# Kernel tuning notes

Measured on AMD Instinct MI355X. Metric: run time of the kernel, lower is better.

## Reference

```python
import jax, jax.numpy as jnp
import numpy as np

N_AGENTS = 12
N_THREADS = 4096
DIM = 3
N_VEC = 4
HID = 64
INV_NF = 32
LAYERS = 2
N = N_THREADS * N_AGENTS


def _intra_graph_edges():
    # fully-connected directed edges within each env's agent graph
    i, j = np.meshgrid(np.arange(N_AGENTS), np.arange(N_AGENTS), indexing='ij')
    mask = i != j
    ri, ci = i[mask], j[mask]  # [132]
    off = (np.arange(N_THREADS) * N_AGENTS)[:, None]
    row = (ri[None, :] + off).reshape(-1).astype(np.int32)
    col = (ci[None, :] + off).reshape(-1).astype(np.int32)
    return jnp.asarray(row), jnp.asarray(col)


def setup_inputs() -> dict:
    key = jax.random.key(0)
    ks = jax.random.split(key, 16)
    s = 0.05
    row, col = _intra_graph_edges()
    return {
        'h0': jax.random.normal(ks[0], (N, INV_NF), jnp.float32),
        'x0': jax.random.normal(ks[1], (N, DIM, N_VEC), jnp.float32),
        'W_embed': jax.random.normal(ks[2], (INV_NF, HID), jnp.float32) * s,
        'b_embed': jnp.zeros((HID,), jnp.float32),
        'We1': jax.random.normal(ks[3], (LAYERS, 2 * HID + N_VEC, HID), jnp.float32) * s,
        'be1': jnp.zeros((LAYERS, HID), jnp.float32),
        'We2': jax.random.normal(ks[4], (LAYERS, HID, HID), jnp.float32) * s,
        'be2': jnp.zeros((LAYERS, HID), jnp.float32),
        'Wx': jax.random.normal(ks[5], (LAYERS, HID, N_VEC), jnp.float32) * s,
        'bx': jnp.zeros((LAYERS, N_VEC), jnp.float32),
        'Wh1': jax.random.normal(ks[6], (LAYERS, 2 * HID, HID), jnp.float32) * s,
        'bh1': jnp.zeros((LAYERS, HID), jnp.float32),
        'Wh2': jax.random.normal(ks[7], (LAYERS, HID, HID), jnp.float32) * s,
        'bh2': jnp.zeros((LAYERS, HID), jnp.float32),
        'w_act': jax.random.normal(ks[8], (N_VEC,), jnp.float32) * s,
        'log_std': jnp.full((DIM,), -0.5, jnp.float32),
        'row': row,
        'col': col,
    }


def reference(h0, x0, W_embed, b_embed, We1, be1, We2, be2, Wx, bx,
              Wh1, bh1, Wh2, bh2, w_act, log_std, row, col):
    silu = jax.nn.silu
    n = h0.shape[0]
    h = h0 @ W_embed + b_embed            # node embedding, [N, HID]
    x = x0                                 # equivariant features, [N, DIM, N_VEC]
    deg = jnp.maximum(jax.ops.segment_sum(jnp.ones_like(row, jnp.float32), row, num_segments=n), 1.0)
    for l in range(LAYERS):
        hi, hj = h[row], h[col]
        diff = x[row] - x[col]                        # [E, DIM, N_VEC]
        radial = jnp.sum(diff * diff, axis=1)          # [E, N_VEC]
        m = silu(jnp.concatenate([hi, hj, radial], -1) @ We1[l] + be1[l])
        m = silu(m @ We2[l] + be2[l])                  # edge messages [E, HID]
        wc = m @ Wx[l] + bx[l]                         # per-vector coord weights [E, N_VEC]
        x = x + jax.ops.segment_sum(diff * wc[:, None, :], row, num_segments=n) / deg[:, None, None]
        agg = jax.ops.segment_sum(m, row, num_segments=n)
        h = h + silu(jnp.concatenate([h, agg], -1) @ Wh1[l] + bh1[l]) @ Wh2[l] + bh2[l]
    mu = jnp.einsum('ndv,v->nd', x, w_act)             # act_net: Linear(N_VEC,1,bias=False)
    actions = mu                                        # deterministic: mode of Normal(mu, std)
    log_probs = jnp.broadcast_to(-log_std - 0.5 * jnp.log(2.0 * jnp.pi), mu.shape)
    actions = actions.reshape(N_THREADS, N_AGENTS, DIM)
    log_probs = log_probs.reshape(N_THREADS, N_AGENTS, DIM)
    return actions, log_probs
```

## Files before the change

### kernel.cpp

```cpp
#include <hip/hip_runtime.h>

#define NAG 12
#define NTH 4096
#define NEDGE 132
#define ENVW 2
#define NWAVE 4
#define LDB 72
#define LDT 20

typedef __bf16 bf16_8 __attribute__((ext_vector_type(8)));
typedef __bf16 bf16_4 __attribute__((ext_vector_type(4)));
typedef float  f32x4  __attribute__((ext_vector_type(4)));

#define MFMA(a,b,c) __builtin_amdgcn_mfma_f32_16x16x32_bf16((a),(b),(c),0,0,0)

#define WS_FRAGS 100
#define WS_BIAS_F32 25600
#define WS_BX_F32   27648
#define WS_BYTES 111104

__device__ __forceinline__ float silu_f(float z) {
    float e = __expf(-z);
    return z * __builtin_amdgcn_rcpf(1.0f + e);
}

__device__ __forceinline__ bf16_8 loadB64(const float* __restrict__ W, int kbase, int n, int q) {
    bf16_8 b;
    #pragma unroll
    for (int j = 0; j < 8; ++j) b[j] = (__bf16)W[(kbase + q*8 + j) * 64 + n];
    return b;
}

__device__ __forceinline__ bf16_8 packA8(const float* S) {
    f32x4 u = *(const f32x4*)S, v = *(const f32x4*)(S + 4);
    bf16_8 a;
    a[0]=(__bf16)u.x; a[1]=(__bf16)u.y; a[2]=(__bf16)u.z; a[3]=(__bf16)u.w;
    a[4]=(__bf16)v.x; a[5]=(__bf16)v.y; a[6]=(__bf16)v.z; a[7]=(__bf16)v.w;
    return a;
}

__global__ __launch_bounds__(64) void prep_frags(
    const float* __restrict__ W_embed, const float* __restrict__ We1,
    const float* __restrict__ We2, const float* __restrict__ Wh1,
    const float* __restrict__ Wh2,
    const float* __restrict__ be1, const float* __restrict__ be2,
    const float* __restrict__ bh1, const float* __restrict__ bh2,
    const float* __restrict__ bx, __bf16* __restrict__ wsb)
{
    const int f = blockIdx.x, lane = threadIdx.x;
    const int q = lane >> 4, n16 = lane & 15;
    float* wsf = (float*)wsb;
    if (f < WS_FRAGS) {
        const float* src; int kbase, nbase;
        if (f < 4) { src = W_embed; kbase = 0; nbase = f * 16; }
        else {
            int g0 = f - 4, l = g0 / 48, r = g0 % 48;
            if      (r < 8)  { int nt=r>>1, kh=r&1;            src = We1 + l*NEDGE*64; kbase = kh*32;      nbase = nt*16; }
            else if (r < 16) { int rr=r-8,  nt=rr>>1, kh=rr&1; src = We1 + l*NEDGE*64; kbase = 64 + kh*32; nbase = nt*16; }
            else if (r < 24) { int rr=r-16, nt=rr>>1, kh=rr&1; src = We2 + l*64*64;    kbase = kh*32;      nbase = nt*16; }
            else if (r < 40) { int rr=r-24, nt=rr>>2, ks=rr&3; src = Wh1 + l*128*64;   kbase = ks*32;      nbase = nt*16; }
            else             { int rr=r-40, nt=rr>>1, kh=rr&1; src = Wh2 + l*64*64;    kbase = kh*32;      nbase = nt*16; }
        }
        bf16_8 b = loadB64(src, kbase, nbase + n16, q);
        *(bf16_8*)(wsb + (size_t)f * 512 + lane * 8) = b;
    } else if (f < WS_FRAGS + 8) {
        int f2 = f - WS_FRAGS, l = f2 >> 2, w = f2 & 3;
        const float* src = (w == 0 ? be1 : w == 1 ? be2 : w == 2 ? bh1 : bh2) + l * 64;
        f32x4 v = { src[n16], src[16 + n16], src[32 + n16], src[48 + n16] };
        *(f32x4*)(wsf + WS_BIAS_F32 + ((size_t)(l*4 + w) * 64 + lane) * 4) = v;
    } else {
        #pragma unroll
        for (int l = 0; l < 2; ++l)
            wsf[WS_BX_F32 + l*64 + lane] = (n16 < 4) ? bx[l*4 + n16] : 0.f;
    }
}

template<bool WS>
__device__ __forceinline__ bf16_8 frg(const __bf16* __restrict__ wsb, int fid,
                                      const float* __restrict__ src, int kbase, int n, int lane) {
    if (WS) return *(const bf16_8*)(wsb + (size_t)fid * 512 + lane * 8);
    else    return loadB64(src, kbase, n, (lane >> 4));
}

template<bool WS>
__global__ void __launch_bounds__(64 * NWAVE) egnn11(
    const float* __restrict__ h0, const float* __restrict__ x0,
    const float* __restrict__ W_embed, const float* __restrict__ b_embed,
    const float* __restrict__ We1, const float* __restrict__ be1,
    const float* __restrict__ We2, const float* __restrict__ be2,
    const float* __restrict__ Wx, const float* __restrict__ bx,
    const float* __restrict__ Wh1, const float* __restrict__ bh1,
    const float* __restrict__ Wh2, const float* __restrict__ bh2,
    const float* __restrict__ w_act, const float* __restrict__ log_std,
    const __bf16* __restrict__ wsb, float* __restrict__ out)
{
    __shared__ __align__(16) __bf16 sh  [NWAVE][ENVW][NAG * LDB];
    __shared__ __align__(16) __bf16 sHa [NWAVE][ENVW][NAG * LDB];
    __shared__ __align__(16) __bf16 sHb [NWAVE][ENVW][NAG * LDB];
    __shared__ __align__(16) __bf16 mstT[NWAVE][ENVW][64 * LDT];
    __shared__ __align__(16) float  sx  [NWAVE][ENVW][NAG * 16];
    __shared__ __align__(16) __bf16 sWcB[NWAVE][ENVW][NEDGE * 4];
    __shared__ __align__(16) float  sWb [NWAVE][4 * 64];

    const int tid  = threadIdx.x;
    const int wv   = tid >> 6;
    const int lane = tid & 63;
    const int q = lane >> 4, n16 = lane & 15;
    const int rowA = (n16 < NAG) ? n16 : (NAG - 1);
    const int env0 = (blockIdx.x * NWAVE + wv) * ENVW;
    const float* wsf = (const float*)wsb;

    if (lane < NAG * 3) {
        int d = lane % 3;
        float lp = -log_std[d] - 0.9189385332046727f;
        #pragma unroll
        for (int ep = 0; ep < ENVW; ++ep)
            out[NTH * NAG * 3 + (env0 + ep) * (NAG*3) + lane] = lp;
    }

    #pragma unroll
    for (int p = 0; p < (ENVW * 144 + 63) / 64; ++p) {
        int idx = p * 64 + lane;
        if (idx < ENVW * 144) {
            int ep = idx / 144, r2 = idx - ep * 144;
            sx[wv][ep][(r2 / 12) * 16 + r2 % 12] = x0[(env0) * NAG * 12 + idx];
        }
    }

    f32x4 hC[ENVW][4];
    {
        bf16_8 a[ENVW];
        #pragma unroll
        for (int ep = 0; ep < ENVW; ++ep)
            a[ep] = packA8(h0 + ((env0 + ep) * NAG + rowA) * 32 + q * 8);
        #pragma unroll
        for (int nt = 0; nt < 4; ++nt) {
            bf16_8 b = frg<WS>(wsb, nt, W_embed, 0, nt*16 + n16, lane);
            float bias = b_embed[nt*16 + n16];
            #pragma unroll
            for (int ep = 0; ep < ENVW; ++ep) {
                f32x4 acc = {0.f,0.f,0.f,0.f};
                acc = MFMA(a[ep], b, acc);
                #pragma unroll
                for (int r = 0; r < 4; ++r) acc[r] += bias;
                hC[ep][nt] = acc;
            }
        }
        #pragma unroll
        for (int ep = 0; ep < ENVW; ++ep)
            #pragma unroll
            for (int nt = 0; nt < 4; ++nt)
                #pragma unroll
                for (int r = 0; r < 4; ++r) {
                    int row = q*4 + r;
                    if (row < NAG) sh[wv][ep][row*LDB + nt*16 + n16] = (__bf16)hC[ep][nt][r];
                }
    }

    #pragma unroll 1
    for (int l = 0; l < 2; ++l) {
        const float* We1l = We1 + l * NEDGE * 64;
        const float* be1l = be1 + l * 64;
        const float* be2l = be2 + l * 64;
        const float* Wxl  = Wx  + l * 64 * 4;
        const float* bxl  = bx  + l * 4;
        const float* We2l = We2 + l * 64 * 64;
        const float* Wh1l = Wh1 + l * 128 * 64;
        const float* bh1l = bh1 + l * 64;
        const float* Wh2l = Wh2 + l * 64 * 64;
        const float* bh2l = bh2 + l * 64;
        const int L = 4 + l * 48;

        f32x4 be1q, be2q, bh1q, bh2q;
        float bxv;
        if (WS) {
            const float* bb = wsf + WS_BIAS_F32 + (size_t)(l*4) * 256 + lane * 4;
            be1q = *(const f32x4*)(bb);
            be2q = *(const f32x4*)(bb + 256);
            bh1q = *(const f32x4*)(bb + 512);
            bh2q = *(const f32x4*)(bb + 768);
            bxv  = wsf[WS_BX_F32 + l*64 + lane];
        } else {
            #pragma unroll
            for (int nt = 0; nt < 4; ++nt) {
                be1q[nt] = be1l[nt*16+n16]; be2q[nt] = be2l[nt*16+n16];
                bh1q[nt] = bh1l[nt*16+n16]; bh2q[nt] = bh2l[nt*16+n16];
            }
            bxv = (n16 < 4) ? bxl[n16] : 0.f;
        }

        {
            bf16_8 a0[ENVW], a1[ENVW];
            #pragma unroll
            for (int ep = 0; ep < ENVW; ++ep) {
                a0[ep] = *(const bf16_8*)(sh[wv][ep] + rowA*LDB + q*8);
                a1[ep] = *(const bf16_8*)(sh[wv][ep] + rowA*LDB + 32 + q*8);
            }
            #pragma unroll
            for (int nt = 0; nt < 4; ++nt) {
                bf16_8 b0 = frg<WS>(wsb, L+nt*2+0,   We1l, 0,  nt*16+n16, lane);
                bf16_8 b1 = frg<WS>(wsb, L+nt*2+1,   We1l, 32, nt*16+n16, lane);
                bf16_8 c0 = frg<WS>(wsb, L+8+nt*2+0, We1l, 64, nt*16+n16, lane);
                bf16_8 c1 = frg<WS>(wsb, L+8+nt*2+1, We1l, 96, nt*16+n16, lane);
                #pragma unroll
                for (int ep = 0; ep < ENVW; ++ep) {
                    f32x4 aA = {0.f,0.f,0.f,0.f}, aB = {0.f,0.f,0.f,0.f};
                    aA = MFMA(a0[ep], b0, aA); aA = MFMA(a1[ep], b1, aA);
                    aB = MFMA(a0[ep], c0, aB); aB = MFMA(a1[ep], c1, aB);
                    #pragma unroll
                    for (int r = 0; r < 4; ++r) {
                        int row = q*4 + r;
                        if (row < NAG) {
                            sHa[wv][ep][row*LDB + nt*16+n16] = (__bf16)(aA[r] + be1q[nt]);
                            sHb[wv][ep][row*LDB + nt*16+n16] = (__bf16)aB[r];
                        }
                    }
                }
            }
        }
        #pragma unroll
        for (int p = 0; p < 4; ++p) sWb[wv][p*64 + lane] = We1l[(128+p)*64 + lane];

        float agg[ENVW][NAG];
        #pragma unroll
        for (int ep = 0; ep < ENVW; ++ep)
            #pragma unroll
            for (int i = 0; i < NAG; ++i) agg[ep][i] = 0.f;
        bf16_8 w2f[4][2], wxf[2];
        #pragma unroll
        for (int nt = 0; nt < 4; ++nt) {
            w2f[nt][0] = frg<WS>(wsb, L+16+nt*2+0, We2l, 0,  nt*16+n16, lane);
            w2f[nt][1] = frg<WS>(wsb, L+16+nt*2+1, We2l, 32, nt*16+n16, lane);
        }
        #pragma unroll
        for (int kh = 0; kh < 2; ++kh) {
            bf16_8 b;
            #pragma unroll
            for (int j2 = 0; j2 < 8; ++j2)
                b[j2] = (n16 < 4) ? (__bf16)Wxl[(kh*32 + q*8 + j2)*4 + n16] : (__bf16)0.f;
            wxf[kh] = b;
        }

        #pragma unroll
        for (int t = 0; t < 9; ++t) {
            const int e  = t*16 + n16;
            const int ec = (e < NEDGE) ? e : (NEDGE - 1);
            const int i  = ec / 11;
            const int jj = ec - i * 11;
            const int j  = jj + (jj >= i);
            bf16_8 af[ENVW][2];
            #pragma unroll
            for (int ep = 0; ep < ENVW; ++ep) {
                f32x4 rd = {0.f,0.f,0.f,0.f};
                #pragma unroll
                for (int d = 0; d < 3; ++d) {
                    f32x4 xi = *(const f32x4*)(sx[wv][ep] + i*16 + d*4);
                    f32x4 xj = *(const f32x4*)(sx[wv][ep] + j*16 + d*4);
                    f32x4 df = xi - xj;
                    rd += df * df;
                }
                #pragma unroll
                for (int kh = 0; kh < 2; ++kh) {
                    const int cb = kh*32 + q*8;
                    bf16_8 ha = *(const bf16_8*)(sHa[wv][ep] + i*LDB + cb);
                    bf16_8 hb = *(const bf16_8*)(sHb[wv][ep] + j*LDB + cb);
                    f32x4 wr0 = {0.f,0.f,0.f,0.f}, wr1 = {0.f,0.f,0.f,0.f};
                    #pragma unroll
                    for (int v = 0; v < 4; ++v) {
                        f32x4 wa = *(const f32x4*)(sWb[wv] + v*64 + cb);
                        f32x4 wb = *(const f32x4*)(sWb[wv] + v*64 + cb + 4);
                        wr0 += rd[v] * wa; wr1 += rd[v] * wb;
                    }
                    bf16_8 a;
                    #pragma unroll
                    for (int c = 0; c < 4; ++c)
                        a[c]   = (__bf16)silu_f((float)ha[c]   + (float)hb[c]   + wr0[c]);
                    #pragma unroll
                    for (int c = 0; c < 4; ++c)
                        a[4+c] = (__bf16)silu_f((float)ha[4+c] + (float)hb[4+c] + wr1[c]);
                    af[ep][kh] = a;
                }
            }
            #pragma unroll
            for (int ep = 0; ep < ENVW; ++ep) {
                __bf16* mT = &mstT[wv][ep][0];
                #pragma unroll
                for (int nt = 0; nt < 4; ++nt) {
                    f32x4 acc = {0.f,0.f,0.f,0.f};
                    acc = MFMA(af[ep][0], w2f[nt][0], acc);
                    acc = MFMA(af[ep][1], w2f[nt][1], acc);
                    bf16_4 mv;
                    #pragma unroll
                    for (int r = 0; r < 4; ++r) mv[r] = (__bf16)silu_f(acc[r] + be2q[nt]);
                    *(bf16_4*)(mT + (nt*16 + n16)*LDT + q*4) = mv;
                }
            }
            #pragma unroll
            for (int ep = 0; ep < ENVW; ++ep) {
                const __bf16* mT = &mstT[wv][ep][0];
                bf16_8 aw0, aw1;
                #pragma unroll
                for (int j2 = 0; j2 < 8; ++j2) {
                    aw0[j2] = mT[(q*8 + j2)*LDT + n16];
                    aw1[j2] = mT[(32 + q*8 + j2)*LDT + n16];
                }
                f32x4 acc = {0.f,0.f,0.f,0.f};
                acc = MFMA(aw0, wxf[0], acc);
                acc = MFMA(aw1, wxf[1], acc);
                if (n16 < 4) {
                    #pragma unroll
                    for (int r = 0; r < 4; ++r) {
                        int row = t*16 + q*4 + r;
                        if (row < NEDGE) sWcB[wv][ep][row*4 + n16] = (__bf16)(acc[r] + bxv);
                    }
                }
            }
            #pragma unroll
            for (int ep = 0; ep < ENVW; ++ep) {
                const __bf16* mT = &mstT[wv][ep][0];
                bf16_4 c0 = *(const bf16_4*)(mT + lane*LDT + 0);
                #pragma unroll
                for (int el = 0; el < 4; ++el) agg[ep][(t*16 + el)/11] += (float)c0[el];
                if (t < 8) {
                    bf16_4 c1 = *(const bf16_4*)(mT + lane*LDT + 4);
                    bf16_4 c2 = *(const bf16_4*)(mT + lane*LDT + 8);
                    bf16_4 c3 = *(const bf16_4*)(mT + lane*LDT + 12);
                    #pragma unroll
                    for (int el = 0; el < 4; ++el) {
                        agg[ep][(t*16 + 4  + el)/11] += (float)c1[el];
                        agg[ep][(t*16 + 8  + el)/11] += (float)c2[el];
                        agg[ep][(t*16 + 12 + el)/11] += (float)c3[el];
                    }
                }
            }
        }
        #pragma unroll
        for (int ep = 0; ep < ENVW; ++ep)
            #pragma unroll
            for (int i = 0; i < NAG; ++i) sHb[wv][ep][i*LDB + lane] = (__bf16)agg[ep][i];

        float xn[ENVW][3];
        #pragma unroll
        for (int p = 0; p < 3; ++p) {
            int idx = p*64 + lane;
            int xi = idx / 12, dv = idx % 12, v = dv & 3;
            bool act = idx < 144;
            int xic = act ? xi : 0;
            #pragma unroll
            for (int ep = 0; ep < ENVW; ++ep) {
                float xiv = sx[wv][ep][xic*16 + dv];
                float acc = 0.f;
                #pragma unroll
                for (int j2 = 0; j2 < NAG; ++j2) {
                    int e2 = xic*11 + j2 - (j2 > xic ? 1 : 0);
                    e2 = (e2 < NEDGE) ? e2 : (NEDGE - 1);
                    float term = (xiv - sx[wv][ep][j2*16 + dv]) * (float)sWcB[wv][ep][e2*4 + v];
                    acc += (j2 == xic) ? 0.f : term;
                }
                xn[ep][p] = act ? (xiv + acc * (1.0f / 11.0f)) : 0.f;
            }
        }
        {
            bf16_8 ah0[ENVW], ah1[ENVW], ag0[ENVW], ag1[ENVW];
            #pragma unroll
            for (int ep = 0; ep < ENVW; ++ep) {
                ah0[ep] = *(const bf16_8*)(sh[wv][ep]  + rowA*LDB + q*8);
                ah1[ep] = *(const bf16_8*)(sh[wv][ep]  + rowA*LDB + 32 + q*8);
                ag0[ep] = *(const bf16_8*)(sHb[wv][ep] + rowA*LDB + q*8);
                ag1[ep] = *(const bf16_8*)(sHb[wv][ep] + rowA*LDB + 32 + q*8);
            }
            #pragma unroll
            for (int nt = 0; nt < 4; ++nt) {
                bf16_8 b0 = frg<WS>(wsb, L+24+nt*4+0, Wh1l, 0,  nt*16+n16, lane);
                bf16_8 b1 = frg<WS>(wsb, L+24+nt*4+1, Wh1l, 32, nt*16+n16, lane);
                bf16_8 b2 = frg<WS>(wsb, L+24+nt*4+2, Wh1l, 64, nt*16+n16, lane);
                bf16_8 b3 = frg<WS>(wsb, L+24+nt*4+3, Wh1l, 96, nt*16+n16, lane);
                #pragma unroll
                for (int ep = 0; ep < ENVW; ++ep) {
                    f32x4 acc = {0.f,0.f,0.f,0.f};
                    acc = MFMA(ah0[ep], b0, acc); acc = MFMA(ah1[ep], b1, acc);
                    acc = MFMA(ag0[ep], b2, acc); acc = MFMA(ag1[ep], b3, acc);
                    #pragma unroll
                    for (int r = 0; r < 4; ++r) {
                        int row = q*4 + r;
                        if (row < NAG) sHa[wv][ep][row*LDB + nt*16+n16] = (__bf16)silu_f(acc[r] + bh1q[nt]);
                    }
                }
            }
        }
        #pragma unroll
        for (int p = 0; p < 3; ++p) {
            int idx = p*64 + lane;
            if (idx < 144) {
                #pragma unroll
                for (int ep = 0; ep < ENVW; ++ep)
                    sx[wv][ep][(idx/12)*16 + idx%12] = xn[ep][p];
            }
        }
        {
            bf16_8 at0[ENVW], at1[ENVW];
            #pragma unroll
            for (int ep = 0; ep < ENVW; ++ep) {
                at0[ep] = *(const bf16_8*)(sHa[wv][ep] + rowA*LDB + q*8);
                at1[ep] = *(const bf16_8*)(sHa[wv][ep] + rowA*LDB + 32 + q*8);
            }
            #pragma unroll
            for (int nt = 0; nt < 4; ++nt) {
                bf16_8 b0 = frg<WS>(wsb, L+40+nt*2+0, Wh2l, 0,  nt*16+n16, lane);
                bf16_8 b1 = frg<WS>(wsb, L+40+nt*2+1, Wh2l, 32, nt*16+n16, lane);
                #pragma unroll
                for (int ep = 0; ep < ENVW; ++ep) {
                    f32x4 acc = {0.f,0.f,0.f,0.f};
                    acc = MFMA(at0[ep], b0, acc);
                    acc = MFMA(at1[ep], b1, acc);
                    #pragma unroll
                    for (int r = 0; r < 4; ++r) hC[ep][nt][r] += acc[r] + bh2q[nt];
                }
            }
            #pragma unroll
            for (int ep = 0; ep < ENVW; ++ep)
                #pragma unroll
                for (int nt = 0; nt < 4; ++nt)
                    #pragma unroll
                    for (int r = 0; r < 4; ++r) {
                        int row = q*4 + r;
                        if (row < NAG) sh[wv][ep][row*LDB + nt*16+n16] = (__bf16)hC[ep][nt][r];
                    }
        }
    }

    if (lane < NAG * 3) {
        int i = lane / 3, d = lane - i * 3;
        #pragma unroll
        for (int ep = 0; ep < ENVW; ++ep) {
            float mu = 0.f;
            #pragma unroll
            for (int v = 0; v < 4; ++v) mu += sx[wv][ep][i*16 + d*4 + v] * w_act[v];
            out[(env0 + ep) * (NAG*3) + lane] = mu;
        }
    }
}

extern "C" void kernel_launch(void* const* d_in, const int* in_sizes, int n_in,
                              void* d_out, int out_size, void* d_ws, size_t ws_size,
                              hipStream_t stream) {
    const float* h0   = (const float*)d_in[0];
    const float* x0   = (const float*)d_in[1];
    const float* Wem  = (const float*)d_in[2];
    const float* bem  = (const float*)d_in[3];
    const float* We1  = (const float*)d_in[4];
    const float* be1  = (const float*)d_in[5];
    const float* We2  = (const float*)d_in[6];
    const float* be2  = (const float*)d_in[7];
    const float* Wx   = (const float*)d_in[8];
    const float* bx   = (const float*)d_in[9];
    const float* Wh1  = (const float*)d_in[10];
    const float* bh1  = (const float*)d_in[11];
    const float* Wh2  = (const float*)d_in[12];
    const float* bh2  = (const float*)d_in[13];
    const float* wact = (const float*)d_in[14];
    const float* lstd = (const float*)d_in[15];
    float* out = (float*)d_out;

    if (ws_size >= (size_t)WS_BYTES) {
        prep_frags<<<dim3(WS_FRAGS + 9), dim3(64), 0, stream>>>(
            Wem, We1, We2, Wh1, Wh2, be1, be2, bh1, bh2, bx, (__bf16*)d_ws);
        egnn11<true><<<dim3(NTH / (ENVW * NWAVE)), dim3(64 * NWAVE), 0, stream>>>(
            h0, x0, Wem, bem, We1, be1, We2, be2, Wx, bx,
            Wh1, bh1, Wh2, bh2, wact, lstd, (const __bf16*)d_ws, out);
    } else {
        egnn11<false><<<dim3(NTH / (ENVW * NWAVE)), dim3(64 * NWAVE), 0, stream>>>(
            h0, x0, Wem, bem, We1, be1, We2, be2, Wx, bx,
            Wh1, bh1, Wh2, bh2, wact, lstd, nullptr, out);
    }
}
```

Before: 222.1 us.

## Aggregate edge messages via MFMA with a one-hot selection matrix

Replaces the per-lane scalar accumulation of edge messages into 12 per-agent registers with an MFMA that multiplies a precomputed one-hot edge-to-node selection fragment by the message tile. Two 16-edge tiles are now processed per step into a widened LDS transpose buffer (LDT doubled) so that each aggregation MFMA covers 32 edges. The unrolled 9-tile loop becomes a non-unrolled 5-iteration loop driven by a macro body. The aim is to cut VALU work and register pressure from the scalar agg array, in exchange for extra LDS, five more workspace fragments and extra MFMA issues.

Measured after the change: 227.2 us. +2.3%, slower.

```diff
diff --git a/kernel.cpp b/kernel.cpp
--- a/kernel.cpp
+++ b/kernel.cpp
@@ -6,7 +6,7 @@
 #define ENVW 2
 #define NWAVE 4
 #define LDB 72
-#define LDT 20
+#define LDT 40
 
 typedef __bf16 bf16_8 __attribute__((ext_vector_type(8)));
 typedef __bf16 bf16_4 __attribute__((ext_vector_type(4)));
@@ -14,10 +14,10 @@
 
 #define MFMA(a,b,c) __builtin_amdgcn_mfma_f32_16x16x32_bf16((a),(b),(c),0,0,0)
 
-#define WS_FRAGS 100
-#define WS_BIAS_F32 25600
-#define WS_BX_F32   27648
-#define WS_BYTES 111104
+#define WS_FRAGS 105
+#define WS_BIAS_F32 26880
+#define WS_BX_F32   28928
+#define WS_BYTES 116224
 
 __device__ __forceinline__ float silu_f(float z) {
     float e = __expf(-z);
@@ -50,7 +50,7 @@
     const int f = blockIdx.x, lane = threadIdx.x;
     const int q = lane >> 4, n16 = lane & 15;
     float* wsf = (float*)wsb;
-    if (f < WS_FRAGS) {
+    if (f < 100) {
         const float* src; int kbase, nbase;
         if (f < 4) { src = W_embed; kbase = 0; nbase = f * 16; }
         else {
@@ -62,6 +62,15 @@
             else             { int rr=r-40, nt=rr>>1, kh=rr&1; src = Wh2 + l*64*64;    kbase = kh*32;      nbase = nt*16; }
         }
         bf16_8 b = loadB64(src, kbase, nbase + n16, q);
+        *(bf16_8*)(wsb + (size_t)f * 512 + lane * 8) = b;
+    } else if (f < WS_FRAGS) {
+        int p = f - 100;
+        bf16_8 b;
+        #pragma unroll
+        for (int j = 0; j < 8; ++j) {
+            int e = p * 32 + q * 8 + j;
+            b[j] = (e < NEDGE && (e / 11) == n16) ? (__bf16)1.0f : (__bf16)0.0f;
+        }
         *(bf16_8*)(wsb + (size_t)f * 512 + lane * 8) = b;
     } else if (f < WS_FRAGS + 8) {
         int f2 = f - WS_FRAGS, l = f2 >> 2, w = f2 & 3;
@@ -221,11 +230,11 @@
         #pragma unroll
         for (int p = 0; p < 4; ++p) sWb[wv][p*64 + lane] = We1l[(128+p)*64 + lane];
 
-        float agg[ENVW][NAG];
+        f32x4 aggC[ENVW][4];
         #pragma unroll
         for (int ep = 0; ep < ENVW; ++ep)
             #pragma unroll
-            for (int i = 0; i < NAG; ++i) agg[ep][i] = 0.f;
+            for (int nt = 0; nt < 4; ++nt) aggC[ep][nt] = (f32x4){0.f,0.f,0.f,0.f};
         bf16_8 w2f[4][2], wxf[2];
         #pragma unroll
         for (int nt = 0; nt < 4; ++nt) {
@@ -241,103 +250,127 @@
             wxf[kh] = b;
         }
 
-        #pragma unroll
-        for (int t = 0; t < 9; ++t) {
-            const int e  = t*16 + n16;
-            const int ec = (e < NEDGE) ? e : (NEDGE - 1);
-            const int i  = ec / 11;
-            const int jj = ec - i * 11;
-            const int j  = jj + (jj >= i);
-            bf16_8 af[ENVW][2];
-            #pragma unroll
-            for (int ep = 0; ep < ENVW; ++ep) {
-                f32x4 rd = {0.f,0.f,0.f,0.f};
-                #pragma unroll
-                for (int d = 0; d < 3; ++d) {
-                    f32x4 xi = *(const f32x4*)(sx[wv][ep] + i*16 + d*4);
-                    f32x4 xj = *(const f32x4*)(sx[wv][ep] + j*16 + d*4);
-                    f32x4 df = xi - xj;
-                    rd += df * df;
-                }
-                #pragma unroll
-                for (int kh = 0; kh < 2; ++kh) {
-                    const int cb = kh*32 + q*8;
-                    bf16_8 ha = *(const bf16_8*)(sHa[wv][ep] + i*LDB + cb);
-                    bf16_8 hb = *(const bf16_8*)(sHb[wv][ep] + j*LDB + cb);
-                    f32x4 wr0 = {0.f,0.f,0.f,0.f}, wr1 = {0.f,0.f,0.f,0.f};
-                    #pragma unroll
-                    for (int v = 0; v < 4; ++v) {
-                        f32x4 wa = *(const f32x4*)(sWb[wv] + v*64 + cb);
-                        f32x4 wb = *(const f32x4*)(sWb[wv] + v*64 + cb + 4);
-                        wr0 += rd[v] * wa; wr1 += rd[v] * wb;
-                    }
-                    bf16_8 a;
-                    #pragma unroll
-                    for (int c = 0; c < 4; ++c)
-                        a[c]   = (__bf16)silu_f((float)ha[c]   + (float)hb[c]   + wr0[c]);
-                    #pragma unroll
-                    for (int c = 0; c < 4; ++c)
-                        a[4+c] = (__bf16)silu_f((float)ha[4+c] + (float)hb[4+c] + wr1[c]);
-                    af[ep][kh] = a;
-                }
-            }
-            #pragma unroll
-            for (int ep = 0; ep < ENVW; ++ep) {
-                __bf16* mT = &mstT[wv][ep][0];
-                #pragma unroll
-                for (int nt = 0; nt < 4; ++nt) {
-                    f32x4 acc = {0.f,0.f,0.f,0.f};
-                    acc = MFMA(af[ep][0], w2f[nt][0], acc);
-                    acc = MFMA(af[ep][1], w2f[nt][1], acc);
-                    bf16_4 mv;
-                    #pragma unroll
-                    for (int r = 0; r < 4; ++r) mv[r] = (__bf16)silu_f(acc[r] + be2q[nt]);
-                    *(bf16_4*)(mT + (nt*16 + n16)*LDT + q*4) = mv;
+#define TILEBODY(T_, HALF_)                                                          \
+        {                                                                            \
+            const int t_ = (T_);                                                     \
+            const int e  = t_*16 + n16;                                              \
+            const int ec = (e < NEDGE) ? e : (NEDGE - 1);                            \
+            const int i  = ec / 11;                                                  \
+            const int jj = ec - i * 11;                                              \
+            const int j  = jj + (jj >= i);                                           \
+            f32x4 rdv[ENVW];                                                         \
+            _Pragma("unroll")                                                        \
+            for (int ep = 0; ep < ENVW; ++ep) {                                      \
+                f32x4 rd = {0.f,0.f,0.f,0.f};                                        \
+                _Pragma("unroll")                                                    \
+                for (int d = 0; d < 3; ++d) {                                        \
+                    f32x4 xi = *(const f32x4*)(sx[wv][ep] + i*16 + d*4);             \
+                    f32x4 xj = *(const f32x4*)(sx[wv][ep] + j*16 + d*4);             \
+                    f32x4 df = xi - xj;                                              \
+                    rd += df * df;                                                   \
+                }                                                                    \
+                rdv[ep] = rd;                                                        \
+            }                                                                        \
+            bf16_8 af[ENVW][2];                                                      \
+            _Pragma("unroll")                                                        \
+            for (int kh = 0; kh < 2; ++kh) {                                         \
+                const int cb = kh*32 + q*8;                                          \
+                f32x4 wa[4], wb[4];                                                  \
+                _Pragma("unroll")                                                    \
+                for (int v = 0; v < 4; ++v) {                                        \
+                    wa[v] = *(const f32x4*)(sWb[wv] + v*64 + cb);                    \
+                    wb[v] = *(const f32x4*)(sWb[wv] + v*64 + cb + 4);                \
+                }                                                                    \
+                _Pragma("unroll")                                                    \
+                for (int ep = 0; ep < ENVW; ++ep) {                                  \
+                    bf16_8 ha = *(const bf16_8*)(sHa[wv][ep] + i*LDB + cb);          \
+                    bf16_8 hb = *(const bf16_8*)(sHb[wv][ep] + j*LDB + cb);          \
+                    f32x4 wr0 = {0.f,0.f,0.f,0.f}, wr1 = {0.f,0.f,0.f,0.f};          \
+                    _Pragma("unroll")                                                \
+                    for (int v = 0; v < 4; ++v) {                                    \
+                        wr0 += rdv[ep][v] * wa[v]; wr1 += rdv[ep][v] * wb[v];        \
+                    }                                                                \
+                    bf16_8 a;                                                        \
+                    _Pragma("unroll")                                                \
+                    for (int c = 0; c < 4; ++c)                                      \
+                        a[c]   = (__bf16)silu_f((float)ha[c]   + (float)hb[c]   + wr0[c]); \
+                    _Pragma("unroll")                                                \
+                    for (int c = 0; c < 4; ++c)                                      \
+                        a[4+c] = (__bf16)silu_f((float)ha[4+c] + (float)hb[4+c] + wr1[c]); \
+                    af[ep][kh] = a;                                                  \
+                }                                                                    \
+            }                                                                        \
+            _Pragma("unroll")                                                        \
+            for (int ep = 0; ep < ENVW; ++ep) {                                      \
+                __bf16* mT = &mstT[wv][ep][0];                                       \
+                _Pragma("unroll")                                                    \
+                for (int nt = 0; nt < 4; ++nt) {                                     \
+                    f32x4 acc = {0.f,0.f,0.f,0.f};                                   \
+                    acc = MFMA(af[ep][0], w2f[nt][0], acc);                          \
+                    acc = MFMA(af[ep][1], w2f[nt][1], acc);                          \
+                    bf16_4 mv;                                                       \
+                    _Pragma("unroll")                                                \
+                    for (int r = 0; r < 4; ++r) mv[r] = (__bf16)silu_f(acc[r] + be2q[nt]); \
+                    *(bf16_4*)(mT + (nt*16 + n16)*LDT + (HALF_)*16 + q*4) = mv;      \
+                }                                                                    \
+            }                                                                        \
+            _Pragma("unroll")                                                        \
+            for (int ep = 0; ep < ENVW; ++ep) {                                      \
+                const __bf16* mT = &mstT[wv][ep][0];                                 \
+                bf16_8 aw0, aw1;                                                     \
+                _Pragma("unroll")                                                    \
+                for (int j2 = 0; j2 < 8; ++j2) {                                     \
+                    aw0[j2] = mT[(q*8 + j2)*LDT + (HALF_)*16 + n16];                 \
+                    aw1[j2] = mT[(32 + q*8 + j2)*LDT + (HALF_)*16 + n16];            \
+                }                                                                    \
+                f32x4 acc = {0.f,0.f,0.f,0.f};                                       \
+                acc = MFMA(aw0, wxf[0], acc);                                        \
+                acc = MFMA(aw1, wxf[1], acc);                                        \
+                if (n16 < 4) {                                                       \
+                    _Pragma("unroll")                                                \
+                    for (int r = 0; r < 4; ++r) {                                    \
+                        int row = t_*16 + q*4 + r;                                   \
+                        if (row < NEDGE) sWcB[wv][ep][row*4 + n16] = (__bf16)(acc[r] + bxv); \
+                    }                                                                \
+                }                                                                    \
+            }                                                                        \
+        }
+
+        #pragma unroll 1
+        for (int p = 0; p < 5; ++p) {
+            TILEBODY(2*p, 0)
+            if (p < 4) { TILEBODY(2*p + 1, 1) }
+            bf16_8 sfr;
+            if (WS) {
+                sfr = *(const bf16_8*)(wsb + (size_t)(100 + p) * 512 + lane * 8);
+            } else {
+                #pragma unroll
+                for (int j2 = 0; j2 < 8; ++j2) {
+                    int e2 = p*32 + q*8 + j2;
+                    sfr[j2] = (e2 < NEDGE && (e2 / 11) == n16) ? (__bf16)1.0f : (__bf16)0.0f;
                 }
             }
             #pragma unroll
             for (int ep = 0; ep < ENVW; ++ep) {
                 const __bf16* mT = &mstT[wv][ep][0];
-                bf16_8 aw0, aw1;
-                #pragma unroll
-                for (int j2 = 0; j2 < 8; ++j2) {
-                    aw0[j2] = mT[(q*8 + j2)*LDT + n16];
-                    aw1[j2] = mT[(32 + q*8 + j2)*LDT + n16];
-                }
-                f32x4 acc = {0.f,0.f,0.f,0.f};
-                acc = MFMA(aw0, wxf[0], acc);
-                acc = MFMA(aw1, wxf[1], acc);
-                if (n16 < 4) {
-                    #pragma unroll
-                    for (int r = 0; r < 4; ++r) {
-                        int row = t*16 + q*4 + r;
-                        if (row < NEDGE) sWcB[wv][ep][row*4 + n16] = (__bf16)(acc[r] + bxv);
-                    }
-                }
-            }
-            #pragma unroll
-            for (int ep = 0; ep < ENVW; ++ep) {
-                const __bf16* mT = &mstT[wv][ep][0];
-                bf16_4 c0 = *(const bf16_4*)(mT + lane*LDT + 0);
-                #pragma unroll
-                for (int el = 0; el < 4; ++el) agg[ep][(t*16 + el)/11] += (float)c0[el];
-                if (t < 8) {
-                    bf16_4 c1 = *(const bf16_4*)(mT + lane*LDT + 4);
-                    bf16_4 c2 = *(const bf16_4*)(mT + lane*LDT + 8);
-                    bf16_4 c3 = *(const bf16_4*)(mT + lane*LDT + 12);
-                    #pragma unroll
-                    for (int el = 0; el < 4; ++el) {
-                        agg[ep][(t*16 + 4  + el)/11] += (float)c1[el];
-                        agg[ep][(t*16 + 8  + el)/11] += (float)c2[el];
-                        agg[ep][(t*16 + 12 + el)/11] += (float)c3[el];
-                    }
-                }
-            }
-        }
+                #pragma unroll
+                for (int nt = 0; nt < 4; ++nt) {
+                    bf16_8 mb = *(const bf16_8*)(mT + (nt*16 + n16)*LDT + q*8);
+                    aggC[ep][nt] = MFMA(sfr, mb, aggC[ep][nt]);
+                }
+            }
+        }
+#undef TILEBODY
+
         #pragma unroll
         for (int ep = 0; ep < ENVW; ++ep)
             #pragma unroll
-            for (int i = 0; i < NAG; ++i) sHb[wv][ep][i*LDB + lane] = (__bf16)agg[ep][i];
+            for (int nt = 0; nt < 4; ++nt)
+                #pragma unroll
+                for (int r = 0; r < 4; ++r) {
+                    int row = q*4 + r;
+                    if (row < NAG) sHb[wv][ep][row*LDB + nt*16+n16] = (__bf16)aggC[ep][nt][r];
+                }
 
         float xn[ENVW][3];
         #pragma unroll
```
